# Optimization experiments

Hardware: AMD Instinct MI355X
Metric: run time of the kernel (lower is better)

The kernel has to match this reference:

```python
import jax, jax.numpy as jnp
import numpy as np

NUM_EMBEDDINGS = 8192
EMBEDDING_DIM = 256
COMMITMENT_COST = 0.25
TEMP = 1.0
EPS_NORM = 1e-12  # torch F.normalize eps


def setup_inputs() -> dict:
    key = jax.random.key(0)
    k1, k2 = jax.random.split(key)
    inputs = jax.random.normal(k1, (16, EMBEDDING_DIM, 32, 32), dtype=jnp.float32)
    emb_weight = jax.random.normal(k2, (NUM_EMBEDDINGS, EMBEDDING_DIM), dtype=jnp.float32) * (1.0 / NUM_EMBEDDINGS)
    return {"inputs": inputs, "emb_weight": emb_weight}


def _l2norm(x):
    n = jnp.sqrt(jnp.sum(x * x, axis=1, keepdims=True))
    return x / jnp.maximum(n, EPS_NORM)


def reference(inputs, emb_weight):
    B, C, H, W = inputs.shape
    K = emb_weight.shape[0]
    x = jnp.transpose(inputs, (0, 2, 3, 1))            # [B,H,W,C]
    flat_x = x.reshape(-1, C)                           # [N,C]
    N = flat_x.shape[0]

    # compute_distances (on L2-normalized vectors), done under no_grad in torch
    fn = _l2norm(flat_x)
    wn = _l2norm(emb_weight)
    distances = (jnp.sum(fn * fn, axis=1, keepdims=True)
                 + jnp.sum(wn * wn, axis=1)
                 - 2.0 * fn @ wn.T)                     # [N,K]

    soft_codes = jax.nn.softmax(-distances / TEMP, axis=-1)  # [N,K]
    encoding_indices = jnp.argmin(distances, axis=-1)        # [N] (stochastic=False)

    # one-hot scatter + matmul == gather of codebook rows
    quantized = emb_weight[encoding_indices].reshape(x.shape)  # [B,H,W,C]

    e_latent_loss = jnp.mean((jax.lax.stop_gradient(quantized) - x) ** 2)
    loss = COMMITMENT_COST * e_latent_loss

    # straight-through
    quantized = x + jax.lax.stop_gradient(quantized - x)
    quantized = jnp.transpose(quantized, (0, 3, 2, 1))  # [B,C,W,H] (as in source)

    # perplexity from one-hot encodings
    counts = jnp.zeros((K,), dtype=jnp.float32).at[encoding_indices].add(1.0)
    avg_probs = counts / N
    perplexity = jnp.exp(-jnp.sum(avg_probs * jnp.log(avg_probs + 1e-10)))

    soft_codes = soft_codes.reshape(B, C, -1)
    return quantized, loss, perplexity, encoding_indices[:, None], soft_codes
```

## Files before the change

### kernel.cpp

```cpp
#include <hip/hip_runtime.h>

#define NPTS   16384
#define KCB    8192
#define CDIM   256
#define HWSZ   1024
#define NB     16

typedef __bf16 bf16;
typedef __bf16 bf16x4v __attribute__((ext_vector_type(4)));
typedef __bf16 bf16x8v __attribute__((ext_vector_type(8)));
typedef float  f32x4v  __attribute__((ext_vector_type(4)));

#define OUT1 4194304
#define OUT2 4194305
#define OUT3 4194306
#define OUT4 4210690

#define MAX_RESCUE 4096
#define ENT_INTS   16

typedef __attribute__((address_space(1))) unsigned int as1_u32;
typedef __attribute__((address_space(3))) unsigned int as3_u32;
__device__ __forceinline__ void glds16(const bf16* g, bf16* l) {
  __builtin_amdgcn_global_load_lds((as1_u32*)(g), (as3_u32*)(l), 16, 0, 0);
}

__global__ void k_norm_emb(const float* __restrict__ emb,
                           bf16* __restrict__ wn_hi, bf16* __restrict__ wn_lo) {
  const int lane = threadIdx.x & 63;
  const int row  = (blockIdx.x << 2) + (threadIdx.x >> 6);
  const float4 v = *(const float4*)(emb + (size_t)row * CDIM + (lane << 2));
  float ss = v.x*v.x + v.y*v.y + v.z*v.z + v.w*v.w;
#pragma unroll
  for (int off = 1; off < 64; off <<= 1) ss += __shfl_xor(ss, off, 64);
  const float inv = 1.0f / fmaxf(sqrtf(ss), 1e-12f);
  const float a0 = v.x*inv, a1 = v.y*inv, a2 = v.z*inv, a3 = v.w*inv;
  const bf16 h0 = (bf16)a0, h1 = (bf16)a1, h2 = (bf16)a2, h3 = (bf16)a3;
  const bf16 l0 = (bf16)(a0 - (float)h0), l1 = (bf16)(a1 - (float)h1),
             l2 = (bf16)(a2 - (float)h2), l3 = (bf16)(a3 - (float)h3);
  *(bf16x4v*)(wn_hi + (size_t)row * CDIM + (lane << 2)) = (bf16x4v){h0, h1, h2, h3};
  *(bf16x4v*)(wn_lo + (size_t)row * CDIM + (lane << 2)) = (bf16x4v){l0, l1, l2, l3};
}

__global__ void k_norm_x(const float* __restrict__ in,
                         bf16* __restrict__ fn_hi, bf16* __restrict__ fn_lo) {
  __shared__ float xs[32][257];
  __shared__ float inv_s[32];
  const int t = threadIdx.x;
  const int b = blockIdx.y;
  const int hw0 = blockIdx.x << 5;
  const int hwo = t & 31, cb = t >> 5;
  const float* src = in + (size_t)b * CDIM * HWSZ + hw0 + hwo;
#pragma unroll
  for (int it = 0; it < 32; ++it) {
    const int c = cb + (it << 3);
    xs[hwo][c] = src[(size_t)c * HWSZ];
  }
  __syncthreads();
  const int wv = t >> 6, lane = t & 63;
#pragma unroll
  for (int j = 0; j < 8; ++j) {
    const int r = wv + (j << 2);
    float ss = 0.f;
#pragma unroll
    for (int e = 0; e < 4; ++e) { const float x = xs[r][lane + (e << 6)]; ss = fmaf(x, x, ss); }
#pragma unroll
    for (int off = 1; off < 64; off <<= 1) ss += __shfl_xor(ss, off, 64);
    if (lane == 0) inv_s[r] = 1.0f / fmaxf(sqrtf(ss), 1e-12f);
  }
  __syncthreads();
#pragma unroll 4
  for (int r = 0; r < 32; ++r) {
    const float v = xs[r][t] * inv_s[r];
    const bf16 h = (bf16)v;
    const bf16 l = (bf16)(v - (float)h);
    const size_t n = (size_t)b * HWSZ + hw0 + r;
    fn_hi[n * CDIM + t] = h;
    fn_lo[n * CDIM + t] = l;
  }
}

__global__ __launch_bounds__(256) void k_gemm(
    const bf16* __restrict__ fn_hi, const bf16* __restrict__ fn_lo,
    const bf16* __restrict__ wn_hi, const bf16* __restrict__ wn_lo,
    float* __restrict__ soft) {
  __shared__ __align__(16) bf16 Ah[128 * 32];
  __shared__ __align__(16) bf16 Al[128 * 32];
  __shared__ __align__(16) bf16 Bh[128 * 32];
  __shared__ __align__(16) bf16 Bl[128 * 32];
  const int t = threadIdx.x;
  const int row0 = blockIdx.y << 7;
  const int col0 = blockIdx.x << 7;
  const int r0 = t >> 2;
  const int cs = (t & 3) << 3;
  const int wv = t >> 6, lane = t & 63;
  const int wm = (wv & 1) << 6, wnn = (wv >> 1) << 6;
  const int ml = lane & 15, quad = lane >> 4;

  const size_t gA0 = (size_t)(row0 + r0) * CDIM + cs;
  const size_t gA1 = gA0 + (size_t)64 * CDIM;
  const size_t gB0 = (size_t)(col0 + r0) * CDIM + cs;
  const size_t gB1 = gB0 + (size_t)64 * CDIM;

  f32x4v acc[4][4] = {};

  for (int c0 = 0; c0 < CDIM; c0 += 32) {
    __syncthreads();
    glds16(fn_hi + gA0 + c0, Ah + t * 8);
    glds16(fn_hi + gA1 + c0, Ah + (t + 256) * 8);
    glds16(fn_lo + gA0 + c0, Al + t * 8);
    glds16(fn_lo + gA1 + c0, Al + (t + 256) * 8);
    glds16(wn_hi + gB0 + c0, Bh + t * 8);
    glds16(wn_hi + gB1 + c0, Bh + (t + 256) * 8);
    glds16(wn_lo + gB0 + c0, Bl + t * 8);
    glds16(wn_lo + gB1 + c0, Bl + (t + 256) * 8);
    __syncthreads();
    bf16x8v ah[4], alo[4], bh[4], blo[4];
#pragma unroll
    for (int i = 0; i < 4; ++i) {
      const int ra = (wm + 16 * i + ml) * 32 + quad * 8;
      const int rb = (wnn + 16 * i + ml) * 32 + quad * 8;
      ah[i]  = *(const bf16x8v*)(Ah + ra);
      alo[i] = *(const bf16x8v*)(Al + ra);
      bh[i]  = *(const bf16x8v*)(Bh + rb);
      blo[i] = *(const bf16x8v*)(Bl + rb);
    }
#pragma unroll
    for (int i = 0; i < 4; ++i)
#pragma unroll
      for (int j = 0; j < 4; ++j) {
        acc[i][j] = __builtin_amdgcn_mfma_f32_16x16x32_bf16(alo[i], bh[j], acc[i][j], 0, 0, 0);
        acc[i][j] = __builtin_amdgcn_mfma_f32_16x16x32_bf16(ah[i], blo[j], acc[i][j], 0, 0, 0);
        acc[i][j] = __builtin_amdgcn_mfma_f32_16x16x32_bf16(ah[i], bh[j], acc[i][j], 0, 0, 0);
      }
  }
#pragma unroll
  for (int i = 0; i < 4; ++i) {
#pragma unroll
    for (int r = 0; r < 4; ++r) {
      const size_t nrow = (size_t)row0 + wm + 16 * i + quad * 4 + r;
      float* dst = soft + nrow * KCB + col0 + wnn + ml;
#pragma unroll
      for (int j = 0; j < 4; ++j)
        dst[16 * j] = __expf(fmaf(2.0f, acc[i][j][r], -2.0f));
    }
  }
}

__global__ __launch_bounds__(256) void k_softnorm(float* __restrict__ soft,
                                                  int* __restrict__ ws_idx,
                                                  int* __restrict__ rescue,
                                                  int* __restrict__ rescue_cnt) {
  const int t = threadIdx.x;
  const size_t n = blockIdx.x;
  float* row = soft + n * (size_t)KCB;
  float2 v[16];
  float sum = 0.f, bp = -1.f;
  int bk = 0;
#pragma unroll
  for (int i = 0; i < 16; ++i) {
    v[i] = *(float2*)(row + i * 512 + t * 2);
    const int k0 = i * 512 + t * 2;
    if (v[i].x > bp) { bp = v[i].x; bk = k0; }
    if (v[i].y > bp) { bp = v[i].y; bk = k0 + 1; }
    sum += v[i].x + v[i].y;
  }
#pragma unroll
  for (int off = 1; off < 64; off <<= 1) {
    sum += __shfl_xor(sum, off, 64);
    const float op = __shfl_xor(bp, off, 64);
    const int   ok = __shfl_xor(bk, off, 64);
    if (op > bp || (op == bp && ok < bk)) { bp = op; bk = ok; }
  }
  __shared__ float s_sum[4], s_bp[4];
  __shared__ int s_bk[4];
  __shared__ int s_cand[16];
  __shared__ int s_ccnt;
  const int wv = t >> 6;
  if (t == 0) s_ccnt = 0;
  if ((t & 63) == 0) { s_sum[wv] = sum; s_bp[wv] = bp; s_bk[wv] = bk; }
  __syncthreads();
  sum = s_sum[0] + s_sum[1] + s_sum[2] + s_sum[3];
  bp = s_bp[0]; bk = s_bk[0];
#pragma unroll
  for (int w2 = 1; w2 < 4; ++w2) {
    const float op = s_bp[w2]; const int ok = s_bk[w2];
    if (op > bp || (op == bp && ok < bk)) { bp = op; bk = ok; }
  }
  const float thr = bp * (1.0f - 5e-4f);
#pragma unroll
  for (int i = 0; i < 16; ++i) {
    if (v[i].x >= thr) { const int p = atomicAdd(&s_ccnt, 1); if (p < 16) s_cand[p] = i * 512 + t * 2; }
    if (v[i].y >= thr) { const int p = atomicAdd(&s_ccnt, 1); if (p < 16) s_cand[p] = i * 512 + t * 2 + 1; }
  }
  __syncthreads();
  if (t == 0) {
    ws_idx[n] = bk;
    int cc = s_ccnt; if (cc > 16) cc = 16;
    if (cc > 1) {
      const int slot = atomicAdd(rescue_cnt, 1);
      if (slot < MAX_RESCUE) {
        int* e = rescue + slot * ENT_INTS;
        const int cn = cc > 14 ? 14 : cc;
        e[0] = (int)n; e[1] = cn;
        for (int j = 0; j < cn; ++j) e[2 + j] = s_cand[j];
      }
    }
  }
  const float inv = 1.0f / sum;
#pragma unroll
  for (int i = 0; i < 16; ++i) {
    v[i].x *= inv; v[i].y *= inv;
    *(float2*)(row + i * 512 + t * 2) = v[i];
  }
}

__global__ __launch_bounds__(256) void k_rescore(const float* __restrict__ in,
                                                 const float* __restrict__ emb,
                                                 const int* __restrict__ rescue,
                                                 const int* __restrict__ rescue_cnt,
                                                 int* __restrict__ ws_idx) {
  __shared__ double sh[4];
  const int t = threadIdx.x;
  int nent = *rescue_cnt; if (nent > MAX_RESCUE) nent = MAX_RESCUE;
  for (int e = blockIdx.x; e < nent; e += gridDim.x) {
    const int* ent = rescue + e * ENT_INTS;
    const int n = ent[0];
    const int cnt = ent[1];
    const int b = n >> 10, hw = n & 1023;
    const double x = (double)in[(size_t)b * (CDIM * HWSZ) + (size_t)t * HWSZ + hw];
    double sx = x * x;
#pragma unroll
    for (int off = 1; off < 64; off <<= 1) sx += __shfl_xor(sx, off, 64);
    if ((t & 63) == 0) sh[t >> 6] = sx;
    __syncthreads();
    sx = sh[0] + sh[1] + sh[2] + sh[3];
    __syncthreads();
    const double xin = 1.0 / fmax(sqrt(sx), 1e-12);
    double bestS = -2.0; int bestk = 0x7fffffff;
    for (int j = 0; j < cnt; ++j) {
      const int k = ent[2 + j];
      const double w = (double)emb[(size_t)k * CDIM + t];
      double sw = w * w, dp = x * w;
#pragma unroll
      for (int off = 1; off < 64; off <<= 1) { sw += __shfl_xor(sw, off, 64); dp += __shfl_xor(dp, off, 64); }
      if ((t & 63) == 0) sh[t >> 6] = sw;
      __syncthreads();
      sw = sh[0] + sh[1] + sh[2] + sh[3];
      __syncthreads();
      if ((t & 63) == 0) sh[t >> 6] = dp;
      __syncthreads();
      dp = sh[0] + sh[1] + sh[2] + sh[3];
      __syncthreads();
      const double s = dp * xin / fmax(sqrt(sw), 1e-12);
      if (s > bestS || (s == bestS && k < bestk)) { bestS = s; bestk = k; }
    }
    if (t == 0) ws_idx[n] = bestk;
  }
}

__global__ void k_hist(const int* __restrict__ ws_idx, float* __restrict__ counts,
                       float* __restrict__ out_idx) {
  const int n = blockIdx.x * 256 + threadIdx.x;
  const int k = ws_idx[n];
  out_idx[n] = (float)k;
  atomicAdd(&counts[k], 1.0f);
}

__global__ void k_quant(const float* __restrict__ emb, const int* __restrict__ ws_idx,
                        float* __restrict__ out0) {
  const int b = blockIdx.x >> 8, c = blockIdx.x & 255;
  const int t = threadIdx.x;
  float* dst = out0 + ((size_t)b * CDIM + c) * HWSZ;
#pragma unroll
  for (int p = t; p < HWSZ; p += 256) {
    const int w = p >> 5, h = p & 31;
    const int n = b * HWSZ + h * 32 + w;
    dst[p] = emb[(size_t)ws_idx[n] * CDIM + c];
  }
}

__global__ void k_loss(const float* __restrict__ in, const float* __restrict__ emb,
                       const int* __restrict__ ws_idx, float* __restrict__ loss_acc) {
  const int t = threadIdx.x, lane = t & 63, wv = t >> 6;
  const int b = blockIdx.x >> 4;
  const int hw = ((blockIdx.x & 15) << 6) + lane;
  const int n = b * HWSZ + hw;
  const float* xp = in + (size_t)b * CDIM * HWSZ + hw;
  const float* ep = emb + (size_t)ws_idx[n] * CDIM;
  float ss = 0.f;
#pragma unroll 8
  for (int cc = 0; cc < 64; ++cc) {
    const int c = (wv << 6) + cc;
    const float d = ep[c] - xp[(size_t)c * HWSZ];
    ss = fmaf(d, d, ss);
  }
#pragma unroll
  for (int off = 1; off < 64; off <<= 1) ss += __shfl_xor(ss, off, 64);
  if (lane == 0) atomicAdd(loss_acc, ss);
}

__global__ void k_final(const float* __restrict__ counts, const float* __restrict__ loss_acc,
                        float* __restrict__ out) {
  const int t = threadIdx.x;
  float s = 0.f;
#pragma unroll
  for (int k = t; k < KCB; k += 256) {
    const float avg = counts[k] * (1.0f / (float)NPTS);
    s += avg * logf(avg + 1e-10f);
  }
#pragma unroll
  for (int off = 1; off < 64; off <<= 1) s += __shfl_xor(s, off, 64);
  __shared__ float sw[4];
  if ((t & 63) == 0) sw[t >> 6] = s;
  __syncthreads();
  if (t == 0) {
    const float S = sw[0] + sw[1] + sw[2] + sw[3];
    out[OUT2] = expf(-S);
    out[OUT1] = 0.25f * loss_acc[0] * (1.0f / 4194304.0f);
  }
}

extern "C" void kernel_launch(void* const* d_in, const int* in_sizes, int n_in,
                              void* d_out, int out_size, void* d_ws, size_t ws_size,
                              hipStream_t stream) {
  const float* inp = (const float*)d_in[0];
  const float* emb = (const float*)d_in[1];
  float* out = (float*)d_out;
  char* ws = (char*)d_ws;

  bf16* wn_hi     = (bf16*)(ws);
  bf16* wn_lo     = (bf16*)(ws + 4194304);
  float* counts   = (float*)(ws + 8388608);
  float* loss_a   = (float*)(ws + 8421376);
  int* rescue_cnt = (int*)(ws + 8421380);
  int* ws_idx     = (int*)(ws + 8421632);
  int* rescue     = (int*)(ws + 8487168);

  bf16* fn_hi = (bf16*)out;
  bf16* fn_lo = ((bf16*)out) + (size_t)NPTS * CDIM;

  (void)hipMemsetAsync(ws + 8388608, 0, 33024, stream);
  k_norm_emb<<<KCB / 4, 256, 0, stream>>>(emb, wn_hi, wn_lo);
  k_norm_x<<<dim3(32, NB), 256, 0, stream>>>(inp, fn_hi, fn_lo);
  k_gemm<<<dim3(KCB / 128, NPTS / 128), 256, 0, stream>>>(fn_hi, fn_lo, wn_hi, wn_lo, out + OUT4);
  k_softnorm<<<NPTS, 256, 0, stream>>>(out + OUT4, ws_idx, rescue, rescue_cnt);
  k_rescore<<<256, 256, 0, stream>>>(inp, emb, rescue, rescue_cnt, ws_idx);
  k_hist<<<NPTS / 256, 256, 0, stream>>>(ws_idx, counts, out + OUT3);
  k_quant<<<NB * CDIM, 256, 0, stream>>>(emb, ws_idx, out);
  k_loss<<<256, 256, 0, stream>>>(inp, emb, ws_idx, loss_a);
  k_final<<<1, 256, 0, stream>>>(counts, loss_a, out);
}
```

Baseline: 1.079 ms.

## Remap GEMM tiles per XCD and use nontemporal stores for soft codes

The 2D GEMM grid becomes a 1D grid whose block id is remapped so that each XCD (bid&7) works on a compact 16x8 super-tile of output tiles. This is meant to improve L2 reuse of the fn/wn operands within each XCD's cache. The 512MB soft-code matrix is now written and read with nontemporal stores and loads in the GEMM and softnorm kernels, to avoid polluting the caches with streaming data. The risk is that nontemporal hints may bypass a cache level that softnorm's reread could otherwise have benefited from.

Result: faster. 982.1 us (-9.0%).

```diff
diff --git a/kernel.cpp b/kernel.cpp
--- a/kernel.cpp
+++ b/kernel.cpp
@@ -10,6 +10,7 @@
 typedef __bf16 bf16x4v __attribute__((ext_vector_type(4)));
 typedef __bf16 bf16x8v __attribute__((ext_vector_type(8)));
 typedef float  f32x4v  __attribute__((ext_vector_type(4)));
+typedef float  f32x2v  __attribute__((ext_vector_type(2)));
 
 #define OUT1 4194304
 #define OUT2 4194305
@@ -89,8 +90,17 @@
   __shared__ __align__(16) bf16 Bh[128 * 32];
   __shared__ __align__(16) bf16 Bl[128 * 32];
   const int t = threadIdx.x;
-  const int row0 = blockIdx.y << 7;
-  const int col0 = blockIdx.x << 7;
+
+  const int bid = blockIdx.x;
+  const int xcd = bid & 7;
+  const int g   = bid >> 3;
+  const int s   = (xcd << 3) + (g >> 7);
+  const int w   = g & 127;
+  const int rowt = ((s >> 3) << 4) + (w >> 3);
+  const int colt = ((s & 7) << 3) + (w & 7);
+  const int row0 = rowt << 7;
+  const int col0 = colt << 7;
+
   const int r0 = t >> 2;
   const int cs = (t & 3) << 3;
   const int wv = t >> 6, lane = t & 63;
@@ -142,7 +152,7 @@
       float* dst = soft + nrow * KCB + col0 + wnn + ml;
 #pragma unroll
       for (int j = 0; j < 4; ++j)
-        dst[16 * j] = __expf(fmaf(2.0f, acc[i][j][r], -2.0f));
+        __builtin_nontemporal_store(__expf(fmaf(2.0f, acc[i][j][r], -2.0f)), dst + 16 * j);
     }
   }
 }
@@ -154,16 +164,16 @@
   const int t = threadIdx.x;
   const size_t n = blockIdx.x;
   float* row = soft + n * (size_t)KCB;
-  float2 v[16];
+  f32x2v v[16];
   float sum = 0.f, bp = -1.f;
   int bk = 0;
 #pragma unroll
   for (int i = 0; i < 16; ++i) {
-    v[i] = *(float2*)(row + i * 512 + t * 2);
+    v[i] = __builtin_nontemporal_load((const f32x2v*)(row + i * 512 + t * 2));
     const int k0 = i * 512 + t * 2;
-    if (v[i].x > bp) { bp = v[i].x; bk = k0; }
-    if (v[i].y > bp) { bp = v[i].y; bk = k0 + 1; }
-    sum += v[i].x + v[i].y;
+    if (v[i][0] > bp) { bp = v[i][0]; bk = k0; }
+    if (v[i][1] > bp) { bp = v[i][1]; bk = k0 + 1; }
+    sum += v[i][0] + v[i][1];
   }
 #pragma unroll
   for (int off = 1; off < 64; off <<= 1) {
@@ -190,8 +200,8 @@
   const float thr = bp * (1.0f - 5e-4f);
 #pragma unroll
   for (int i = 0; i < 16; ++i) {
-    if (v[i].x >= thr) { const int p = atomicAdd(&s_ccnt, 1); if (p < 16) s_cand[p] = i * 512 + t * 2; }
-    if (v[i].y >= thr) { const int p = atomicAdd(&s_ccnt, 1); if (p < 16) s_cand[p] = i * 512 + t * 2 + 1; }
+    if (v[i][0] >= thr) { const int p = atomicAdd(&s_ccnt, 1); if (p < 16) s_cand[p] = i * 512 + t * 2; }
+    if (v[i][1] >= thr) { const int p = atomicAdd(&s_ccnt, 1); if (p < 16) s_cand[p] = i * 512 + t * 2 + 1; }
   }
   __syncthreads();
   if (t == 0) {
@@ -210,8 +220,8 @@
   const float inv = 1.0f / sum;
 #pragma unroll
   for (int i = 0; i < 16; ++i) {
-    v[i].x *= inv; v[i].y *= inv;
-    *(float2*)(row + i * 512 + t * 2) = v[i];
+    v[i][0] *= inv; v[i][1] *= inv;
+    __builtin_nontemporal_store(v[i], (f32x2v*)(row + i * 512 + t * 2));
   }
 }
 
@@ -343,7 +353,7 @@
   (void)hipMemsetAsync(ws + 8388608, 0, 33024, stream);
   k_norm_emb<<<KCB / 4, 256, 0, stream>>>(emb, wn_hi, wn_lo);
   k_norm_x<<<dim3(32, NB), 256, 0, stream>>>(inp, fn_hi, fn_lo);
-  k_gemm<<<dim3(KCB / 128, NPTS / 128), 256, 0, stream>>>(fn_hi, fn_lo, wn_hi, wn_lo, out + OUT4);
+  k_gemm<<<8192, 256, 0, stream>>>(fn_hi, fn_lo, wn_hi, wn_lo, out + OUT4);
   k_softnorm<<<NPTS, 256, 0, stream>>>(out + OUT4, ws_idx, rescue, rescue_cnt);
   k_rescore<<<256, 256, 0, stream>>>(inp, emb, rescue, rescue_cnt, ws_idx);
   k_hist<<<NPTS / 256, 256, 0, stream>>>(ws_idx, counts, out + OUT3);
```
